# Optimization experiments

Measured on AMD Instinct MI355X. Metric: run time of the kernel, lower is better.

The kernel has to match this reference:

```python
import jax, jax.numpy as jnp
import numpy as np

HEAD_DIM = 256
N_Q = 8
N_KV = 4
HIDDEN = 2304
WINDOW = 1024
SOFT_CAP = 50.0
MAX_WAVELENGTH = 10000.0


def _rope(x, start_index=0):
    # x: [b, s, n, h]. keras_hub RotaryEmbedding (rotate-half convention),
    # followed by Gemma's interleave permutation of the feature dim.
    b, s, n, h = x.shape
    inv_freq = 1.0 / (MAX_WAVELENGTH ** (jnp.arange(0, h, 2, dtype=jnp.float32) / h))
    pos = jnp.arange(s, dtype=jnp.float32) + start_index
    freq = pos[:, None] * inv_freq[None, :]            # [s, h/2]
    emb = jnp.concatenate([freq, freq], axis=-1)[None, :, None, :]  # [1, s, 1, h]
    cos, sin = jnp.cos(emb).astype(x.dtype), jnp.sin(emb).astype(x.dtype)
    x1, x2 = jnp.split(x, 2, axis=-1)
    rot = jnp.concatenate([-x2, x1], axis=-1)
    y = x * cos + rot * sin
    # Gemma _apply_rope: split halves then interleave (same permutation on q and k)
    a, b2 = jnp.split(y, 2, axis=-1)
    return jnp.stack([a, b2], axis=-1).reshape(x.shape)


def setup_inputs() -> dict:
    key = jax.random.key(0)
    ks = jax.random.split(key, 5)
    B, T, D = 2, 2048, HIDDEN
    x = jax.random.normal(ks[0], (B, T, D), dtype=jnp.float32)
    # causal mask [b, q_len, kv_len]
    causal = jnp.tril(jnp.ones((T, T), dtype=bool))
    attention_mask = jnp.broadcast_to(causal[None], (B, T, T))
    scale = 0.02
    Wq = jax.random.normal(ks[1], (N_Q, D, HEAD_DIM), dtype=jnp.float32) * scale
    Wk = jax.random.normal(ks[2], (N_KV, D, HEAD_DIM), dtype=jnp.float32) * scale
    Wv = jax.random.normal(ks[3], (N_KV, D, HEAD_DIM), dtype=jnp.float32) * scale
    Wo = jax.random.normal(ks[4], (N_Q, HEAD_DIM, D), dtype=jnp.float32) * scale
    return {"x": x, "attention_mask": attention_mask, "Wq": Wq, "Wk": Wk, "Wv": Wv, "Wo": Wo}


def reference(x, attention_mask, Wq, Wk, Wv, Wo):
    b, t, d = x.shape
    q = jnp.einsum('btd,ndh->btnh', x, Wq)
    k = jnp.einsum('bsd,kdh->bskh', x, Wk)
    v = jnp.einsum('bsd,kdh->bskh', x, Wv)
    q = _rope(q)
    k = _rope(k)
    s = k.shape[1]
    # sliding window band mask (triu(-w+1) & tril(w-1)), rows sliced at cache_update_index=0
    i = jnp.arange(s)[:, None]
    j = jnp.arange(s)[None, :]
    sliding = (j - i <= WINDOW - 1) & (i - j <= WINDOW - 1)
    mask = attention_mask & sliding[None, :t, :s]      # [b, t, s]
    q = q * jnp.asarray(1.0 / np.sqrt(HEAD_DIM), dtype=q.dtype)
    g = N_Q // N_KV
    qg = q.reshape(b, t, N_KV, g, HEAD_DIM)
    logits = jnp.einsum('btkgh,bskh->bkgts', qg, k).astype(jnp.float32)
    logits = jnp.tanh(logits / SOFT_CAP) * SOFT_CAP    # logit soft-cap
    m = mask[:, None, None, :, :]                      # [b, 1, 1, t, s]
    logits = jnp.where(m, logits, jnp.float32(-1e30))
    probs = jax.nn.softmax(logits, axis=-1).astype(q.dtype)
    out = jnp.einsum('bkgts,bskh->btkgh', probs, v).reshape(b, t, N_Q, HEAD_DIM)
    no_attended = jnp.all(~attention_mask, axis=-1, keepdims=True)[..., None]  # [b, t, 1, 1]
    out = jnp.where(no_attended, jnp.zeros_like(out), out)
    return jnp.einsum('btnh,nhd->btd', out, Wo)
```

## Files before the change

### kernel.cpp

```cpp
#include <hip/hip_runtime.h>
#include <math.h>

#define HEAD_DIM 256
#define N_Q 8
#define N_KV 4
#define HIDDEN 2304
#define WINDOW 1024
#define BATCH 2
#define SEQ 2048
#define BT (BATCH*SEQ)

typedef unsigned short u16;
typedef __attribute__((ext_vector_type(8))) short bf16x8;
typedef __attribute__((ext_vector_type(4))) float f32x4;

__device__ __forceinline__ u16 f2bf(float f) {
    union { float f; unsigned u; } c; c.f = f;
    unsigned r = c.u + 0x7FFF + ((c.u >> 16) & 1);
    return (u16)(r >> 16);
}
__device__ __forceinline__ float bf2f(u16 b) {
    union { float f; unsigned u; } c; c.u = ((unsigned)b) << 16;
    return c.f;
}

__global__ __launch_bounds__(256) void convert_x_kernel(
    const float* __restrict__ x, u16* __restrict__ xb, int n8)
{
    int i = blockIdx.x * 256 + threadIdx.x;
    if (i >= n8) return;
    const float4 a = ((const float4*)x)[2*i];
    const float4 b = ((const float4*)x)[2*i+1];
    u16 o[8] = { f2bf(a.x), f2bf(a.y), f2bf(a.z), f2bf(a.w),
                 f2bf(b.x), f2bf(b.y), f2bf(b.z), f2bf(b.w) };
    ((uint4*)xb)[i] = *(const uint4*)o;
}

__global__ __launch_bounds__(256) void wqkv_t_kernel(
    const float* __restrict__ Wq, const float* __restrict__ Wk,
    const float* __restrict__ Wv, u16* __restrict__ Wt)
{
    __shared__ float t[64][65];
    const int j = blockIdx.z;
    const float* W = (j < 8)  ? Wq + (size_t)j*HIDDEN*HEAD_DIM
                   : (j < 12) ? Wk + (size_t)(j-8)*HIDDEN*HEAD_DIM
                              : Wv + (size_t)(j-12)*HIDDEN*HEAD_DIM;
    const int d0 = blockIdx.x * 64, h0 = blockIdx.y * 64;
    const int tid = threadIdx.x;
    {
        const int r = tid >> 4, c4 = tid & 15;
        #pragma unroll
        for (int rr = r; rr < 64; rr += 16) {
            const float4 v = *(const float4*)(W + (size_t)(d0+rr)*HEAD_DIM + h0 + c4*4);
            t[rr][c4*4+0] = v.x; t[rr][c4*4+1] = v.y;
            t[rr][c4*4+2] = v.z; t[rr][c4*4+3] = v.w;
        }
    }
    __syncthreads();
    {
        const int hh = tid >> 2;
        #pragma unroll
        for (int it = 0; it < 2; it++) {
            const int chunk = (tid & 3) + it*4;
            u16 tmp[8];
            #pragma unroll
            for (int jj = 0; jj < 8; jj++) tmp[jj] = f2bf(t[chunk*8+jj][hh]);
            *(uint4*)&Wt[(size_t)(j*256 + h0 + hh)*HIDDEN + d0 + chunk*8] = *(const uint4*)tmp;
        }
    }
}

__global__ __launch_bounds__(256) void wo_t_kernel(
    const float* __restrict__ Wo, u16* __restrict__ Wot)
{
    __shared__ float t[64][65];
    const int k0 = blockIdx.x * 64, d0 = blockIdx.y * 64;
    const int tid = threadIdx.x;
    {
        const int r = tid >> 4, c4 = tid & 15;
        #pragma unroll
        for (int rr = r; rr < 64; rr += 16) {
            const float4 v = *(const float4*)(Wo + (size_t)(k0+rr)*HIDDEN + d0 + c4*4);
            t[rr][c4*4+0] = v.x; t[rr][c4*4+1] = v.y;
            t[rr][c4*4+2] = v.z; t[rr][c4*4+3] = v.w;
        }
    }
    __syncthreads();
    {
        const int dd = tid >> 2;
        #pragma unroll
        for (int it = 0; it < 2; it++) {
            const int chunk = (tid & 3) + it*4;
            u16 tmp[8];
            #pragma unroll
            for (int jj = 0; jj < 8; jj++) tmp[jj] = f2bf(t[chunk*8+jj][dd]);
            *(uint4*)&Wot[(size_t)(d0 + dd)*(N_Q*HEAD_DIM) + k0 + chunk*8] = *(const uint4*)tmp;
        }
    }
}

template<typename OutT>
__global__ __launch_bounds__(256) void gemm_bf16_kernel(
    const u16* __restrict__ A, const u16* __restrict__ Bt,
    OutT* __restrict__ C, int M, int N, int K)
{
    __shared__ u16 As[128*64];
    __shared__ u16 Bs[128*64];
    const int m0 = blockIdx.y * 128;
    const int n0 = blockIdx.x * 128;
    const int tid  = threadIdx.x;
    const int lane = tid & 63;
    const int wave = tid >> 6;
    const int wm = (wave & 1) * 64;
    const int wn = (wave >> 1) * 64;
    const int l16  = lane & 15;
    const int quad = lane >> 4;

    const int srow8  = lane >> 3;
    const int schunk = (lane & 7) ^ srow8;
    const u16* Ag = A  + (size_t)(m0 + wave*8 + srow8)*K + schunk*8;
    const u16* Bg = Bt + (size_t)(n0 + wave*8 + srow8)*K + schunk*8;

    const int axor = l16 & 7;
    const u16* ArA = As + (wm + l16)*64;
    const u16* BrB = Bs + (wn + l16)*64;

    f32x4 acc[4][4];
    #pragma unroll
    for (int i = 0; i < 4; i++)
        #pragma unroll
        for (int j = 0; j < 4; j++) acc[i][j] = (f32x4){0.f,0.f,0.f,0.f};

    for (int k0 = 0; k0 < K; k0 += 64) {
        __syncthreads();
        #pragma unroll
        for (int c = 0; c < 4; c++) {
            __builtin_amdgcn_global_load_lds(
                (const __attribute__((address_space(1))) unsigned int*)(Ag + (size_t)c*32*K + k0),
                (__attribute__((address_space(3))) unsigned int*)&As[(c*32 + wave*8)*64],
                16, 0, 0);
            __builtin_amdgcn_global_load_lds(
                (const __attribute__((address_space(1))) unsigned int*)(Bg + (size_t)c*32*K + k0),
                (__attribute__((address_space(3))) unsigned int*)&Bs[(c*32 + wave*8)*64],
                16, 0, 0);
        }
        __syncthreads();
        #pragma unroll
        for (int kk = 0; kk < 2; kk++) {
            bf16x8 af[4], bfr[4];
            #pragma unroll
            for (int t = 0; t < 4; t++)
                af[t]  = *(const bf16x8*)(ArA + t*16*64 + (((kk<<2)|quad) ^ axor)*8);
            #pragma unroll
            for (int t = 0; t < 4; t++)
                bfr[t] = *(const bf16x8*)(BrB + t*16*64 + (((kk<<2)|quad) ^ axor)*8);
            #pragma unroll
            for (int i = 0; i < 4; i++)
                #pragma unroll
                for (int j = 0; j < 4; j++)
                    acc[i][j] = __builtin_amdgcn_mfma_f32_16x16x32_bf16(
                                    af[i], bfr[j], acc[i][j], 0, 0, 0);
        }
    }

    #pragma unroll
    for (int i = 0; i < 4; i++) {
        const int rbase = m0 + wm + i*16 + quad*4;
        #pragma unroll
        for (int j = 0; j < 4; j++) {
            const int col = n0 + wn + j*16 + l16;
            #pragma unroll
            for (int r = 0; r < 4; r++) {
                const float v = acc[i][j][r];
                if constexpr (sizeof(OutT) == 2)
                    ((u16*)C)[(size_t)(rbase + r)*N + col] = f2bf(v);
                else
                    ((float*)C)[(size_t)(rbase + r)*N + col] = v;
            }
        }
    }
}

template<int KK>
__device__ __forceinline__ void g256_ld_b(const u16 (&BsB)[16384], bf16x8 (&bf)[4],
                                          int wcol, int l16, int quad, int axor)
{
    #pragma unroll
    for (int j = 0; j < 4; j++)
        bf[j] = *(const bf16x8*)(&BsB[(wcol*64 + j*16 + l16)*64 + (((KK<<2)|quad)^axor)*8]);
}
template<int MH, int KK>
__device__ __forceinline__ void g256_ld_a(const u16 (&AsB)[16384], bf16x8 (&af)[4],
                                          int wrow, int l16, int quad, int axor)
{
    #pragma unroll
    for (int i = 0; i < 4; i++)
        af[i] = *(const bf16x8*)(&AsB[(wrow*128 + MH*64 + i*16 + l16)*64 + (((KK<<2)|quad)^axor)*8]);
}
template<int MH>
__device__ __forceinline__ void g256_mfma(const bf16x8 (&af)[4], const bf16x8 (&bf)[4],
                                          f32x4 (&acc)[8][4])
{
    __builtin_amdgcn_s_setprio(1);
    #pragma unroll
    for (int i = 0; i < 4; i++)
        #pragma unroll
        for (int j = 0; j < 4; j++)
            acc[MH*4+i][j] = __builtin_amdgcn_mfma_f32_16x16x32_bf16(
                                 af[i], bf[j], acc[MH*4+i][j], 0, 0, 0);
    __builtin_amdgcn_s_setprio(0);
}

#define STG256(DST, SRCP, R0, KT)                                              \
    __builtin_amdgcn_global_load_lds(                                          \
        (const __attribute__((address_space(1))) unsigned int*)                \
            ((SRCP) + (size_t)(R0)*K + (size_t)(KT)*64),                       \
        (__attribute__((address_space(3))) unsigned int*)                      \
            (&DST[((R0) + wave*8)*64]),                                        \
        16, 0, 0)

template<typename OutT>
__global__ __launch_bounds__(512, 2) void gemm256_kernel(
    const u16* __restrict__ A, const u16* __restrict__ Bt,
    OutT* __restrict__ C, int M, int N, int K)
{
    __shared__ __align__(16) u16 As0[16384];
    __shared__ __align__(16) u16 As1[16384];
    __shared__ __align__(16) u16 Bs0[16384];
    __shared__ __align__(16) u16 Bs1[16384];

    const int nwg = gridDim.x;
    const int bid = blockIdx.x;
    const int cpx = nwg >> 3;
    const int swz = (bid & 7) * cpx + (bid >> 3);
    const int NX  = N >> 8;
    const int m0  = (swz / NX) << 8;
    const int n0  = (swz % NX) << 8;

    const int tid  = threadIdx.x;
    const int lane = tid & 63;
    const int wave = tid >> 6;
    const int wrow = wave >> 2;
    const int wcol = wave & 3;
    const int l16  = lane & 15;
    const int quad = lane >> 4;
    const int axor = l16 & 7;

    const int srow8  = lane >> 3;
    const int schunk = (lane & 7) ^ srow8;
    const u16* Ag = A  + (size_t)(m0 + wave*8 + srow8)*K + schunk*8;
    const u16* Bg = Bt + (size_t)(n0 + wave*8 + srow8)*K + schunk*8;

    f32x4 acc[8][4];
    #pragma unroll
    for (int i = 0; i < 8; i++)
        #pragma unroll
        for (int j = 0; j < 4; j++) acc[i][j] = (f32x4){0.f,0.f,0.f,0.f};
    bf16x8 af[4], bf[4];

    #pragma unroll
    for (int h = 0; h < 4; h++) STG256(As0, Ag, h*64, 0);
    #pragma unroll
    for (int h = 0; h < 4; h++) STG256(Bs0, Bg, h*64, 0);
    #pragma unroll
    for (int h = 0; h < 4; h++) STG256(As1, Ag, h*64, 1);
    #pragma unroll
    for (int h = 0; h < 4; h++) STG256(Bs1, Bg, h*64, 1);
    asm volatile("s_waitcnt vmcnt(8)" ::: "memory");
    __builtin_amdgcn_s_barrier();

    const int NT2 = K >> 7;
    for (int t = 0; t < NT2; ++t) {
        const int T1 = 2*t+1, T2 = 2*t+2, T3 = 2*t+3;
        const bool nf = (t > 0);
        const bool nl = (t < NT2-1);

        g256_ld_b<0>(Bs0, bf, wcol, l16, quad, axor);
        g256_ld_a<0,0>(As0, af, wrow, l16, quad, axor);
        if (nf) { STG256(Bs1, Bg, 128, T1); STG256(Bs1, Bg, 192, T1); }
        __builtin_amdgcn_s_barrier();
        g256_mfma<0>(af, bf, acc);
        __builtin_amdgcn_s_barrier();

        g256_ld_a<1,0>(As0, af, wrow, l16, quad, axor);
        if (nf) { STG256(As1, Ag, 0, T1); STG256(As1, Ag, 64, T1); }
        __builtin_amdgcn_s_barrier();
        g256_mfma<1>(af, bf, acc);
        __builtin_amdgcn_s_barrier();

        g256_ld_b<1>(Bs0, bf, wcol, l16, quad, axor);
        g256_ld_a<0,1>(As0, af, wrow, l16, quad, axor);
        if (nf) { STG256(As1, Ag, 128, T1); STG256(As1, Ag, 192, T1); }
        __builtin_amdgcn_s_barrier();
        g256_mfma<0>(af, bf, acc);
        __builtin_amdgcn_s_barrier();

        g256_ld_a<1,1>(As0, af, wrow, l16, quad, axor);
        if (nl) { STG256(Bs0, Bg, 0, T2); STG256(Bs0, Bg, 64, T2); }
        __builtin_amdgcn_s_barrier();
        g256_mfma<1>(af, bf, acc);
        if (nl) asm volatile("s_waitcnt vmcnt(2)" ::: "memory");
        else    asm volatile("s_waitcnt vmcnt(0)" ::: "memory");
        __builtin_amdgcn_s_barrier();

        g256_ld_b<0>(Bs1, bf, wcol, l16, quad, axor);
        g256_ld_a<0,0>(As1, af, wrow, l16, quad, axor);
        if (nl) { STG256(Bs0, Bg, 128, T2); STG256(Bs0, Bg, 192, T2); }
        __builtin_amdgcn_s_barrier();
        g256_mfma<0>(af, bf, acc);
        __builtin_amdgcn_s_barrier();

        g256_ld_a<1,0>(As1, af, wrow, l16, quad, axor);
        if (nl) { STG256(As0, Ag, 0, T2); STG256(As0, Ag, 64, T2); }
        __builtin_amdgcn_s_barrier();
        g256_mfma<1>(af, bf, acc);
        __builtin_amdgcn_s_barrier();

        g256_ld_b<1>(Bs1, bf, wcol, l16, quad, axor);
        g256_ld_a<0,1>(As1, af, wrow, l16, quad, axor);
        if (nl) { STG256(As0, Ag, 128, T2); STG256(As0, Ag, 192, T2); }
        __builtin_amdgcn_s_barrier();
        g256_mfma<0>(af, bf, acc);
        __builtin_amdgcn_s_barrier();

        g256_ld_a<1,1>(As1, af, wrow, l16, quad, axor);
        if (nl) { STG256(Bs1, Bg, 0, T3); STG256(Bs1, Bg, 64, T3); }
        __builtin_amdgcn_s_barrier();
        g256_mfma<1>(af, bf, acc);
        if (nl) asm volatile("s_waitcnt vmcnt(2)" ::: "memory");
        __builtin_amdgcn_s_barrier();
    }

    #pragma unroll
    for (int ii = 0; ii < 8; ii++) {
        const int rbase = m0 + wrow*128 + ii*16 + quad*4;
        #pragma unroll
        for (int j = 0; j < 4; j++) {
            const int col = n0 + wcol*64 + j*16 + l16;
            #pragma unroll
            for (int r = 0; r < 4; r++) {
                const float v = acc[ii][j][r];
                if constexpr (sizeof(OutT) == 2)
                    ((u16*)C)[(size_t)(rbase + r)*N + col] = f2bf(v);
                else
                    ((float*)C)[(size_t)(rbase + r)*N + col] = v;
            }
        }
    }
}

__global__ __launch_bounds__(256) void rope_kernel(
    const u16* __restrict__ raw, u16* __restrict__ qb, u16* __restrict__ kbf)
{
    const int r   = blockIdx.x;
    const int pos = r & (SEQ-1);
    const int tid = threadIdx.x;
    const u16* row = raw + (size_t)r * 4096;
    const float LOG1E4 = 9.210340371976184f;

    #pragma unroll
    for (int p = tid; p < 1024; p += 256) {
        const int n = p >> 7, j = p & 127;
        const float lo = bf2f(row[n*256 + j]);
        const float hi = bf2f(row[n*256 + j + 128]);
        const float inv = __expf(-LOG1E4 * (float)j * (1.0f/128.0f));
        float s, c; sincosf((float)pos * inv, &s, &c);
        qb[((size_t)r*N_Q + n)*HEAD_DIM + j]       = f2bf((lo*c - hi*s) * 0.0625f);
        qb[((size_t)r*N_Q + n)*HEAD_DIM + j + 128] = f2bf((hi*c + lo*s) * 0.0625f);
    }
    #pragma unroll
    for (int p = tid; p < 512; p += 256) {
        const int n = p >> 7, j = p & 127;
        const float lo = bf2f(row[2048 + n*256 + j]);
        const float hi = bf2f(row[2048 + n*256 + j + 128]);
        const float inv = __expf(-LOG1E4 * (float)j * (1.0f/128.0f));
        float s, c; sincosf((float)pos * inv, &s, &c);
        kbf[((size_t)r*N_KV + n)*HEAD_DIM + j]       = f2bf(lo*c - hi*s);
        kbf[((size_t)r*N_KV + n)*HEAD_DIM + j + 128] = f2bf(hi*c + lo*s);
    }
}

__global__ __launch_bounds__(256) void vtrans_kernel(
    const u16* __restrict__ raw, u16* __restrict__ vtt)
{
    __shared__ u16 T[32*264];
    const int blk = blockIdx.x;
    const int sc  = blk & 63;
    const int bk  = blk >> 6;
    const int b   = bk >> 2, kh = bk & 3;
    const int tid = threadIdx.x;

    const u16* rrow = raw + (size_t)(b*SEQ + sc*32)*4096 + 3072 + kh*256;
    {
        const int s = tid >> 3;
        #pragma unroll
        for (int it = 0; it < 4; it++) {
            const int seg = (tid & 7) + it*8;
            *(uint4*)&T[s*264 + seg*8] = *(const uint4*)(rrow + (size_t)s*4096 + seg*8);
        }
    }
    __syncthreads();
    u16* out = vtt + (size_t)blk*8192;
    #pragma unroll
    for (int it = 0; it < 4; it++) {
        const int o = tid + it*256;
        const int h = o >> 2, ss = o & 3;
        u16 tmp[8];
        #pragma unroll
        for (int j = 0; j < 8; j++) tmp[j] = T[(ss*8 + j)*264 + h];
        *(uint4*)(out + h*32 + ((ss ^ (h & 3))*8)) = *(const uint4*)tmp;
    }
}

#define AQT 64
__global__ __launch_bounds__(256) void attn_mfma_kernel(
    const u16* __restrict__ qb, const u16* __restrict__ kb,
    const u16* __restrict__ vtt, u16* __restrict__ ao)
{
    __shared__ u16 Ks[32*264];
    __shared__ u16 Vs[256*32];
    __shared__ u16 Ps[64*40];
    __shared__ float lsum[64];

    const int qh = blockIdx.y;
    const int kh = qh >> 1;
    const int bx = ((blockIdx.y >> 2) & 1) ? (gridDim.x - 1 - (int)blockIdx.x)
                                           : (int)blockIdx.x;
    const int t0 = bx * AQT;
    const int b  = t0 >> 11;
    const int tb = t0 & (SEQ-1);
    const int tid  = threadIdx.x;
    const int wave = tid >> 6;
    const int lane = tid & 63;
    const int l16  = lane & 15;
    const int quad = lane >> 4;

    bf16x8 qf[8];
    {
        const u16* qrow = qb + ((size_t)(t0 + wave*16 + l16)*N_Q + qh)*HEAD_DIM + quad*8;
        #pragma unroll
        for (int c = 0; c < 8; c++) qf[c] = *(const bf16x8*)(qrow + c*32);
    }

    f32x4 o[4][4];
    #pragma unroll
    for (int i = 0; i < 4; i++)
        #pragma unroll
        for (int j = 0; j < 4; j++) o[i][j] = (f32x4){0.f,0.f,0.f,0.f};
    float lpart[4] = {0.f, 0.f, 0.f, 0.f};

    int s_begin = tb - (WINDOW-1); if (s_begin < 0) s_begin = 0;
    const int st0 = s_begin & ~31;

    const u16* kbase = kb  + ((size_t)(b*SEQ)*N_KV + kh)*HEAD_DIM;
    const u16* vbase = vtt + ((size_t)(b*N_KV + kh)*SEQ)*HEAD_DIM;

    for (int st = st0; st < tb + AQT; st += 32) {
        __syncthreads();
        {
            const u16* vtile = vbase + (size_t)st*HEAD_DIM;
            #pragma unroll
            for (int c = 0; c < 4; c++) {
                const int off = wave*2048 + c*512;
                __builtin_amdgcn_global_load_lds(
                    (const __attribute__((address_space(1))) unsigned int*)(vtile + off + lane*8),
                    (__attribute__((address_space(3))) unsigned int*)&Vs[off],
                    16, 0, 0);
            }
            const int s = tid >> 3;
            const u16* krow = kbase + (size_t)(st + s)*(N_KV*HEAD_DIM);
            #pragma unroll
            for (int it = 0; it < 4; it++) {
                const int seg = (tid & 7) + it*8;
                *(uint4*)&Ks[s*264 + seg*8] = *(const uint4*)(krow + seg*8);
            }
        }
        __syncthreads();

        f32x4 sc[2];
        #pragma unroll
        for (int sf = 0; sf < 2; sf++) {
            f32x4 a = (f32x4){0.f,0.f,0.f,0.f};
            const u16* kr = &Ks[(sf*16 + l16)*264 + quad*8];
            #pragma unroll
            for (int c = 0; c < 8; c++)
                a = __builtin_amdgcn_mfma_f32_16x16x32_bf16(
                        qf[c], *(const bf16x8*)(kr + c*32), a, 0, 0, 0);
            sc[sf] = a;
        }

        #pragma unroll
        for (int sf = 0; sf < 2; sf++) {
            const int sg = st + sf*16 + l16;
            #pragma unroll
            for (int r = 0; r < 4; r++) {
                const int tg = tb + wave*16 + quad*4 + r;
                const float e1 = __expf(sc[sf][r] * 0.04f);
                float p = __expf(-100.0f / (e1 + 1.0f));
                const bool ok = (sg <= tg) && (tg - sg < WINDOW);
                p = ok ? p : 0.0f;
                lpart[r] += p;
                Ps[(wave*16 + quad*4 + r)*40 + sf*16 + l16] = f2bf(p);
            }
        }
        __syncthreads();

        bf16x8 ap[4];
        #pragma unroll
        for (int i = 0; i < 4; i++)
            ap[i] = *(const bf16x8*)&Ps[(i*16 + l16)*40 + quad*8];
        #pragma unroll
        for (int j = 0; j < 4; j++) {
            const int hr = wave*64 + j*16 + l16;
            const bf16x8 bv = *(const bf16x8*)&Vs[hr*32 + ((quad ^ (l16 & 3))*8)];
            #pragma unroll
            for (int i = 0; i < 4; i++)
                o[i][j] = __builtin_amdgcn_mfma_f32_16x16x32_bf16(ap[i], bv, o[i][j], 0, 0, 0);
        }
    }

    #pragma unroll
    for (int r = 0; r < 4; r++) {
        float s = lpart[r];
        #pragma unroll
        for (int sh = 1; sh <= 8; sh <<= 1) s += __shfl_xor(s, sh, 64);
        if (l16 == 0) lsum[wave*16 + quad*4 + r] = s;
    }
    __syncthreads();

    #pragma unroll
    for (int i = 0; i < 4; i++) {
        #pragma unroll
        for (int r = 0; r < 4; r++) {
            const int rl  = i*16 + quad*4 + r;
            const float inv = 1.0f / (lsum[rl] + 1e-30f);
            u16* arow = ao + ((size_t)(t0 + rl)*N_Q + qh)*HEAD_DIM + wave*64 + l16;
            #pragma unroll
            for (int j = 0; j < 4; j++)
                arow[j*16] = f2bf(o[i][j][r] * inv);
        }
    }
}

extern "C" void kernel_launch(void* const* d_in, const int* in_sizes, int n_in,
                              void* d_out, int out_size, void* d_ws, size_t ws_size,
                              hipStream_t stream)
{
    const float* x  = (const float*)d_in[0];
    const float* Wq = (const float*)d_in[2];
    const float* Wk = (const float*)d_in[3];
    const float* Wv = (const float*)d_in[4];
    const float* Wo = (const float*)d_in[5];
    float* out = (float*)d_out;

    char* w = (char*)d_ws;
    u16* qbuf = (u16*)(w);
    u16* kbuf = (u16*)(w +  16777216ull);
    u16* vtt  = (u16*)(w +  25165824ull);
    u16* aob  = (u16*)(w +  33554432ull);
    u16* xb   = (u16*)(w +  50331648ull);
    u16* wt1  = (u16*)(w +  69206016ull);
    u16* wot  = (u16*)(w +  88080384ull);
    u16* raw  = (u16*)(w +  97517568ull);

    const int n8 = BT*HIDDEN/8;
    convert_x_kernel<<<(n8+255)/256, 256, 0, stream>>>(x, xb, n8);
    wqkv_t_kernel<<<dim3(HIDDEN/64, HEAD_DIM/64, 16), 256, 0, stream>>>(Wq, Wk, Wv, wt1);
    wo_t_kernel<<<dim3(N_Q*HEAD_DIM/64, HIDDEN/64), 256, 0, stream>>>(Wo, wot);

    gemm256_kernel<u16><<<(BT/256)*(4096/256), 512, 0, stream>>>(
        xb, wt1, raw, BT, 4096, HIDDEN);
    rope_kernel<<<BT, 256, 0, stream>>>(raw, qbuf, kbuf);
    vtrans_kernel<<<BATCH*N_KV*64, 256, 0, stream>>>(raw, vtt);
    attn_mfma_kernel<<<dim3(BT/AQT, N_Q), 256, 0, stream>>>(qbuf, kbuf, vtt, aob);
    gemm_bf16_kernel<float><<<dim3(HIDDEN/128, BT/128), 256, 0, stream>>>(
        aob, wot, out, BT, HIDDEN, N_Q*HEAD_DIM);
}
```

Before: 388.4 us.

## Use pipelined 256-tile GEMM for output projection and rebalance prefetch schedule

```diff
diff --git a/kernel.cpp b/kernel.cpp
--- a/kernel.cpp
+++ b/kernel.cpp
@@ -99,88 +99,6 @@
     }
 }
 
-template<typename OutT>
-__global__ __launch_bounds__(256) void gemm_bf16_kernel(
-    const u16* __restrict__ A, const u16* __restrict__ Bt,
-    OutT* __restrict__ C, int M, int N, int K)
-{
-    __shared__ u16 As[128*64];
-    __shared__ u16 Bs[128*64];
-    const int m0 = blockIdx.y * 128;
-    const int n0 = blockIdx.x * 128;
-    const int tid  = threadIdx.x;
-    const int lane = tid & 63;
-    const int wave = tid >> 6;
-    const int wm = (wave & 1) * 64;
-    const int wn = (wave >> 1) * 64;
-    const int l16  = lane & 15;
-    const int quad = lane >> 4;
-
-    const int srow8  = lane >> 3;
-    const int schunk = (lane & 7) ^ srow8;
-    const u16* Ag = A  + (size_t)(m0 + wave*8 + srow8)*K + schunk*8;
-    const u16* Bg = Bt + (size_t)(n0 + wave*8 + srow8)*K + schunk*8;
-
-    const int axor = l16 & 7;
-    const u16* ArA = As + (wm + l16)*64;
-    const u16* BrB = Bs + (wn + l16)*64;
-
-    f32x4 acc[4][4];
-    #pragma unroll
-    for (int i = 0; i < 4; i++)
-        #pragma unroll
-        for (int j = 0; j < 4; j++) acc[i][j] = (f32x4){0.f,0.f,0.f,0.f};
-
-    for (int k0 = 0; k0 < K; k0 += 64) {
-        __syncthreads();
-        #pragma unroll
-        for (int c = 0; c < 4; c++) {
-            __builtin_amdgcn_global_load_lds(
-                (const __attribute__((address_space(1))) unsigned int*)(Ag + (size_t)c*32*K + k0),
-                (__attribute__((address_space(3))) unsigned int*)&As[(c*32 + wave*8)*64],
-                16, 0, 0);
-            __builtin_amdgcn_global_load_lds(
-                (const __attribute__((address_space(1))) unsigned int*)(Bg + (size_t)c*32*K + k0),
-                (__attribute__((address_space(3))) unsigned int*)&Bs[(c*32 + wave*8)*64],
-                16, 0, 0);
-        }
-        __syncthreads();
-        #pragma unroll
-        for (int kk = 0; kk < 2; kk++) {
-            bf16x8 af[4], bfr[4];
-            #pragma unroll
-            for (int t = 0; t < 4; t++)
-                af[t]  = *(const bf16x8*)(ArA + t*16*64 + (((kk<<2)|quad) ^ axor)*8);
-            #pragma unroll
-            for (int t = 0; t < 4; t++)
-                bfr[t] = *(const bf16x8*)(BrB + t*16*64 + (((kk<<2)|quad) ^ axor)*8);
-            #pragma unroll
-            for (int i = 0; i < 4; i++)
-                #pragma unroll
-                for (int j = 0; j < 4; j++)
-                    acc[i][j] = __builtin_amdgcn_mfma_f32_16x16x32_bf16(
-                                    af[i], bfr[j], acc[i][j], 0, 0, 0);
-        }
-    }
-
-    #pragma unroll
-    for (int i = 0; i < 4; i++) {
-        const int rbase = m0 + wm + i*16 + quad*4;
-        #pragma unroll
-        for (int j = 0; j < 4; j++) {
-            const int col = n0 + wn + j*16 + l16;
-            #pragma unroll
-            for (int r = 0; r < 4; r++) {
-                const float v = acc[i][j][r];
-                if constexpr (sizeof(OutT) == 2)
-                    ((u16*)C)[(size_t)(rbase + r)*N + col] = f2bf(v);
-                else
-                    ((float*)C)[(size_t)(rbase + r)*N + col] = v;
-            }
-        }
-    }
-}
-
 template<int KK>
 __device__ __forceinline__ void g256_ld_b(const u16 (&BsB)[16384], bf16x8 (&bf)[4],
                                           int wcol, int l16, int quad, int axor)
@@ -218,6 +136,9 @@
         (__attribute__((address_space(3))) unsigned int*)                      \
             (&DST[((R0) + wave*8)*64]),                                        \
         16, 0, 0)
+
+#define WAITV(N) asm volatile("s_waitcnt vmcnt(" #N ")" ::: "memory")
+#define BAR()    __builtin_amdgcn_s_barrier()
 
 template<typename OutT>
 __global__ __launch_bounds__(512, 2) void gemm256_kernel(
@@ -258,77 +179,75 @@
         for (int j = 0; j < 4; j++) acc[i][j] = (f32x4){0.f,0.f,0.f,0.f};
     bf16x8 af[4], bf[4];
 
-    #pragma unroll
-    for (int h = 0; h < 4; h++) STG256(As0, Ag, h*64, 0);
-    #pragma unroll
-    for (int h = 0; h < 4; h++) STG256(Bs0, Bg, h*64, 0);
-    #pragma unroll
-    for (int h = 0; h < 4; h++) STG256(As1, Ag, h*64, 1);
-    #pragma unroll
-    for (int h = 0; h < 4; h++) STG256(Bs1, Bg, h*64, 1);
-    asm volatile("s_waitcnt vmcnt(8)" ::: "memory");
-    __builtin_amdgcn_s_barrier();
+    STG256(Bs0, Bg,   0, 0); STG256(Bs0, Bg,  64, 0);
+    STG256(Bs0, Bg, 128, 0); STG256(Bs0, Bg, 192, 0);
+    STG256(As0, Ag,   0, 0); STG256(As0, Ag, 128, 0);
+    STG256(As0, Ag,  64, 0); STG256(As0, Ag, 192, 0);
+    STG256(Bs1, Bg,   0, 1); STG256(Bs1, Bg,  64, 1);
+    WAITV(4);
+    BAR();
 
     const int NT2 = K >> 7;
     for (int t = 0; t < NT2; ++t) {
         const int T1 = 2*t+1, T2 = 2*t+2, T3 = 2*t+3;
-        const bool nf = (t > 0);
         const bool nl = (t < NT2-1);
 
         g256_ld_b<0>(Bs0, bf, wcol, l16, quad, axor);
         g256_ld_a<0,0>(As0, af, wrow, l16, quad, axor);
-        if (nf) { STG256(Bs1, Bg, 128, T1); STG256(Bs1, Bg, 192, T1); }
-        __builtin_amdgcn_s_barrier();
+        STG256(Bs1, Bg, 128, T1); STG256(Bs1, Bg, 192, T1);
+        BAR();
         g256_mfma<0>(af, bf, acc);
-        __builtin_amdgcn_s_barrier();
+        WAITV(4);
+        BAR();
 
         g256_ld_a<1,0>(As0, af, wrow, l16, quad, axor);
-        if (nf) { STG256(As1, Ag, 0, T1); STG256(As1, Ag, 64, T1); }
-        __builtin_amdgcn_s_barrier();
+        STG256(As1, Ag, 0, T1); STG256(As1, Ag, 128, T1);
+        BAR();
         g256_mfma<1>(af, bf, acc);
-        __builtin_amdgcn_s_barrier();
+        BAR();
 
         g256_ld_b<1>(Bs0, bf, wcol, l16, quad, axor);
         g256_ld_a<0,1>(As0, af, wrow, l16, quad, axor);
-        if (nf) { STG256(As1, Ag, 128, T1); STG256(As1, Ag, 192, T1); }
-        __builtin_amdgcn_s_barrier();
+        STG256(As1, Ag, 64, T1); STG256(As1, Ag, 192, T1);
+        BAR();
         g256_mfma<0>(af, bf, acc);
-        __builtin_amdgcn_s_barrier();
+        BAR();
 
         g256_ld_a<1,1>(As0, af, wrow, l16, quad, axor);
         if (nl) { STG256(Bs0, Bg, 0, T2); STG256(Bs0, Bg, 64, T2); }
-        __builtin_amdgcn_s_barrier();
+        BAR();
         g256_mfma<1>(af, bf, acc);
-        if (nl) asm volatile("s_waitcnt vmcnt(2)" ::: "memory");
-        else    asm volatile("s_waitcnt vmcnt(0)" ::: "memory");
-        __builtin_amdgcn_s_barrier();
+        if (nl) { WAITV(4); }
+        else    { WAITV(0); }
+        BAR();
 
         g256_ld_b<0>(Bs1, bf, wcol, l16, quad, axor);
         g256_ld_a<0,0>(As1, af, wrow, l16, quad, axor);
         if (nl) { STG256(Bs0, Bg, 128, T2); STG256(Bs0, Bg, 192, T2); }
-        __builtin_amdgcn_s_barrier();
+        BAR();
         g256_mfma<0>(af, bf, acc);
-        __builtin_amdgcn_s_barrier();
+        WAITV(4);
+        BAR();
 
         g256_ld_a<1,0>(As1, af, wrow, l16, quad, axor);
-        if (nl) { STG256(As0, Ag, 0, T2); STG256(As0, Ag, 64, T2); }
-        __builtin_amdgcn_s_barrier();
+        if (nl) { STG256(As0, Ag, 0, T2); STG256(As0, Ag, 128, T2); }
+        BAR();
         g256_mfma<1>(af, bf, acc);
-        __builtin_amdgcn_s_barrier();
+        BAR();
 
         g256_ld_b<1>(Bs1, bf, wcol, l16, quad, axor);
         g256_ld_a<0,1>(As1, af, wrow, l16, quad, axor);
-        if (nl) { STG256(As0, Ag, 128, T2); STG256(As0, Ag, 192, T2); }
-        __builtin_amdgcn_s_barrier();
+        if (nl) { STG256(As0, Ag, 64, T2); STG256(As0, Ag, 192, T2); }
+        BAR();
         g256_mfma<0>(af, bf, acc);
-        __builtin_amdgcn_s_barrier();
+        BAR();
 
         g256_ld_a<1,1>(As1, af, wrow, l16, quad, axor);
         if (nl) { STG256(Bs1, Bg, 0, T3); STG256(Bs1, Bg, 64, T3); }
-        __builtin_amdgcn_s_barrier();
+        BAR();
         g256_mfma<1>(af, bf, acc);
-        if (nl) asm volatile("s_waitcnt vmcnt(2)" ::: "memory");
-        __builtin_amdgcn_s_barrier();
+        WAITV(4);
+        BAR();
     }
 
     #pragma unroll
@@ -573,6 +492,6 @@
     rope_kernel<<<BT, 256, 0, stream>>>(raw, qbuf, kbuf);
     vtrans_kernel<<<BATCH*N_KV*64, 256, 0, stream>>>(raw, vtt);
     attn_mfma_kernel<<<dim3(BT/AQT, N_Q), 256, 0, stream>>>(qbuf, kbuf, vtt, aob);
-    gemm_bf16_kernel<float><<<dim3(HIDDEN/128, BT/128), 256, 0, stream>>>(
+    gemm256_kernel<float><<<(BT/256)*(HIDDEN/256), 512, 0, stream>>>(
         aob, wot, out, BT, HIDDEN, N_Q*HEAD_DIM);
 }
```

Measured after the change: 372.7 us. -4.0%, faster.
